# Performance work log

Hardware: AMD Instinct MI355X
Metric: run time of the kernel (lower is better)

## Reference

```python
import jax, jax.numpy as jnp
import numpy as np

N_W, N_E, N_UP, N_DN = 4096, 32, 16, 16
D, N_LAYERS, K_DET = 64, 3, 16
BOX = 6.0


def _ln(x, g, b, eps=1e-5):
    mu = x.mean(-1, keepdims=True)
    v = ((x - mu) ** 2).mean(-1, keepdims=True)
    return (x - mu) / jnp.sqrt(v + eps) * g + b


def setup_inputs() -> dict:
    key = jax.random.key(0)
    ks = jax.random.split(key, 24)
    f32 = jnp.float32

    def w(k, shape, s=0.1):
        return (jax.random.normal(k, shape) * s).astype(f32)

    cell = (BOX * jnp.eye(3)).astype(f32)
    twist = w(ks[0], (3,), 0.3)
    r_electrons = (jax.random.uniform(ks[1], (N_W, N_E, 3)) * BOX).astype(f32)
    inp = dict(
        r_electrons=r_electrons, cell=cell, twist=twist,
        W_e=w(ks[2], (3, D)), b_e=w(ks[3], (D,), 0.05),
        W_pw=w(ks[4], (6, D)), b_pw=w(ks[5], (D,), 0.05),
        W1=w(ks[6], (N_LAYERS, 3 * D, D)), b1=w(ks[7], (N_LAYERS, D), 0.05),
        W2=w(ks[8], (N_LAYERS, D, D)), b2=w(ks[9], (N_LAYERS, D), 0.05),
        ln_w=jnp.ones((N_LAYERS, D), f32), ln_b=jnp.zeros((N_LAYERS, D), f32),
        W_up=w(ks[10], (D, K_DET * N_UP)), b_up=w(ks[11], (K_DET * N_UP,), 0.05),
        W_dn=w(ks[12], (D, K_DET * N_DN)), b_dn=w(ks[13], (K_DET * N_DN,), 0.05),
        det_weights=jnp.zeros((K_DET,), f32),
        Wj1=w(ks[14], (1, 32)), bj1=w(ks[15], (32,), 0.05),
        Wj2=w(ks[16], (32, 32)), bj2=w(ks[17], (32,), 0.05),
        Wj3=w(ks[18], (32, 1)), bj3=w(ks[19], (1,), 0.05),
        jastrow_scale=jnp.asarray(0.1, f32),
    )
    return inp


def reference(r_electrons, cell, twist, W_e, b_e, W_pw, b_pw, W1, b1, W2, b2,
              ln_w, ln_b, W_up, b_up, W_dn, b_dn, det_weights,
              Wj1, bj1, Wj2, bj2, Wj3, bj3, jastrow_scale):
    L_inv = jnp.linalg.inv(cell)
    # wrap to cell via fractional coords
    s = r_electrons @ L_inv.T
    r = (s - jnp.floor(s)) @ cell  # [Nw, Ne, 3]
    # plane-wave features on wrapped positions
    s2 = r @ L_inv.T
    two_pi = 2.0 * jnp.pi
    pw = jnp.concatenate([jnp.sin(two_pi * s2), jnp.cos(two_pi * s2)], axis=-1)
    h = r @ W_e + b_e + pw @ W_pw + b_pw  # [Nw, Ne, D]
    # mean-field interaction layers
    for l in range(W1.shape[0]):
        hm = jnp.broadcast_to(h.mean(axis=1, keepdims=True), h.shape)
        x = jnp.concatenate([h, hm, h * hm], axis=-1)  # [Nw, Ne, 3D]
        delta = jax.nn.silu(x @ W1[l] + b1[l]) @ W2[l] + b2[l]
        h = _ln(h + delta, ln_w[l], ln_b[l])
    # minimum-image pairwise distances
    d = r[:, :, None, :] - r[:, None, :, :]  # [Nw, Ne, Ne, 3]
    sij = d @ L_inv.T
    vec = (sij - jnp.round(sij)) @ cell
    r_ij = jnp.linalg.norm(vec, axis=-1)  # [Nw, Ne, Ne]
    iu, ju = np.triu_indices(r.shape[1], 1)
    rp = r_ij[:, iu, ju][..., None]  # [Nw, P, 1]
    j = jax.nn.silu(rp @ Wj1 + bj1)
    j = jax.nn.silu(j @ Wj2 + bj2)
    j = (j @ Wj3 + bj3)[..., 0]
    jastrow = jastrow_scale * j.sum(axis=1)  # [Nw]
    # multi-determinant combine (vectorized over K via signed logsumexp)
    K = det_weights.shape[0]
    n_up = W_up.shape[1] // K
    n_dn = W_dn.shape[1] // K
    orb_up = h[:, :n_up] @ W_up + b_up  # [Nw, n_up, K*n_up]
    phi_up = jnp.moveaxis(orb_up.reshape(-1, n_up, K, n_up), 2, 1)  # [Nw,K,n_up,n_up]
    su, lu = jnp.linalg.slogdet(phi_up)
    orb_dn = h[:, n_up:] @ W_dn + b_dn
    phi_dn = jnp.moveaxis(orb_dn.reshape(-1, n_dn, K, n_dn), 2, 1)
    sd, ld = jnp.linalg.slogdet(phi_dn)
    logs = lu + ld + jnp.log(jax.nn.softmax(det_weights) + 1e-10)[None, :]  # [Nw,K]
    signs = su * sd
    m = jnp.max(logs, axis=1, keepdims=True)
    ssum = jnp.sum(signs * jnp.exp(logs - m), axis=1)
    log_psi = jastrow + m[:, 0] + jnp.log(jnp.abs(ssum) + 1e-30)
    sign_psi = jnp.sign(ssum)
    return log_psi, sign_psi
```

## Files before the change

kernel.cpp:

```cpp
#include <hip/hip_runtime.h>

#define N_WALK 4096
#define N_EL   32
#define DIM    64
#define HPAD   68
#define NLAY   3
#define KDET   16
#define NPAIR  496
#define TWO_PI_D 6.283185307179586476925286766559
#define JTAB_N    8192
#define JTAB_RMAX 5.25f

using f64x4 = __attribute__((ext_vector_type(4))) double;

#define MFMA64(A, B, C) __builtin_amdgcn_mfma_f64_16x16x4f64((A), (B), (C), 0, 0, 0)

__device__ __forceinline__ double exp_d(double x) {
  const double LOG2E  = 1.4426950408889634074;
  const double LN2_HI = 6.93147180369123816490e-01;
  const double LN2_LO = 1.90821492927058770002e-10;
  const double nf = rint(x * LOG2E);
  double r = fma(-nf, LN2_HI, x);
  r = fma(-nf, LN2_LO, r);
  double p = 1.0/3628800.0;
  p = fma(p, r, 1.0/362880.0);
  p = fma(p, r, 1.0/40320.0);
  p = fma(p, r, 1.0/5040.0);
  p = fma(p, r, 1.0/720.0);
  p = fma(p, r, 1.0/120.0);
  p = fma(p, r, 1.0/24.0);
  p = fma(p, r, 1.0/6.0);
  p = fma(p, r, 0.5);
  p = fma(p, r, 1.0);
  p = fma(p, r, 1.0);
  const long long bits = ((long long)((int)nf + 1023)) << 52;
  return p * __longlong_as_double(bits);
}

__device__ __forceinline__ double silu_d(double x) {
  const double d = 1.0 + exp_d(-x);
  const double q0 = (double)(1.0f / (float)d);
  double q = q0 * (2.0 - d * q0);
  q = q * (2.0 - d * q);
  return x * q;
}
__device__ __forceinline__ float silu_q(float x) { return x / (1.0f + __expf(-x)); }

__global__ __launch_bounds__(256) void jtab_kernel(
    const float* __restrict__ Wj1, const float* __restrict__ bj1,
    const float* __restrict__ Wj2, const float* __restrict__ bj2,
    const float* __restrict__ Wj3, const float* __restrict__ bj3,
    float* __restrict__ tab)
{
  const int i = blockIdx.x * 256 + threadIdx.x;
  if (i > JTAB_N) return;
  const float r = (float)i * (JTAB_RMAX / (float)JTAB_N);
  float h1[32];
  #pragma unroll
  for (int m=0;m<32;m++) h1[m] = silu_q(fmaf(r, Wj1[m], bj1[m]));
  float o = bj3[0];
  for (int n=0;n<32;n++) {
    float a2 = bj2[n];
    #pragma unroll
    for (int m=0;m<32;m++) a2 = fmaf(h1[m], Wj2[m*32+n], a2);
    o = fmaf(silu_q(a2), Wj3[n], o);
  }
  tab[i] = o;
}

__global__ __launch_bounds__(256) void wf_kernel(
    const float* __restrict__ r_el,
    const float* __restrict__ cell,
    const float* __restrict__ W_e,  const float* __restrict__ b_e,
    const float* __restrict__ W_pw, const float* __restrict__ b_pw,
    const float* __restrict__ W1,   const float* __restrict__ b1,
    const float* __restrict__ W2,   const float* __restrict__ b2,
    const float* __restrict__ ln_w, const float* __restrict__ ln_b,
    const float* __restrict__ W_up, const float* __restrict__ b_up,
    const float* __restrict__ W_dn, const float* __restrict__ b_dn,
    const float* __restrict__ det_w,
    const float* __restrict__ jtab,
    const float* __restrict__ jscale,
    float* __restrict__ out)
{
  __shared__ float s_linv[9];
  __shared__ float s_cl[9];
  __shared__ float s_r[N_EL][3];
  __shared__ float s_pw[N_EL][6];
  __shared__ float s_h[N_EL][HPAD];
  __shared__ float s_u[16*257];
  __shared__ float s_hm[DIM];
  __shared__ double s_hb[DIM];
  __shared__ double s_lu[2][KDET];
  __shared__ float  s_su[2][KDET];
  __shared__ float  s_red[4];
#define SY(e,d)   s_u[(e)*HPAD + (d)]
#define SORB(j,c) s_u[(j)*257 + (c)]

  const int t = threadIdx.x;
  const int w = blockIdx.x;
  const int wv = t >> 6;
  const int l  = t & 63;
  const int lr = l & 15;
  const int lq = l >> 4;

  if (t == 0) {
    double m00=cell[0], m01=cell[1], m02=cell[2];
    double m10=cell[3], m11=cell[4], m12=cell[5];
    double m20=cell[6], m21=cell[7], m22=cell[8];
    double c00 = m11*m22 - m12*m21;
    double c10 = m12*m20 - m10*m22;
    double c20 = m10*m21 - m11*m20;
    double det = m00*c00 + m01*c10 + m02*c20;
    double id = 1.0/det;
    s_linv[0]=(float)(c00*id); s_linv[1]=(float)((m02*m21-m01*m22)*id); s_linv[2]=(float)((m01*m12-m02*m11)*id);
    s_linv[3]=(float)(c10*id); s_linv[4]=(float)((m00*m22-m02*m20)*id); s_linv[5]=(float)((m02*m10-m00*m12)*id);
    s_linv[6]=(float)(c20*id); s_linv[7]=(float)((m01*m20-m00*m21)*id); s_linv[8]=(float)((m00*m11-m01*m10)*id);
    #pragma unroll
    for (int i=0;i<9;i++) s_cl[i]=cell[i];
  }
  __syncthreads();

  if (t < N_EL) {
    const float* rp = r_el + ((size_t)w * N_EL + t) * 3;
    const float rx = rp[0], ry = rp[1], rz = rp[2];
    float s0 = (float)((double)s_linv[0]*rx + (double)s_linv[1]*ry + (double)s_linv[2]*rz);
    float s1 = (float)((double)s_linv[3]*rx + (double)s_linv[4]*ry + (double)s_linv[5]*rz);
    float s2 = (float)((double)s_linv[6]*rx + (double)s_linv[7]*ry + (double)s_linv[8]*rz);
    s0 -= floorf(s0); s1 -= floorf(s1); s2 -= floorf(s2);
    const float wx = (float)((double)s0*s_cl[0] + (double)s1*s_cl[3] + (double)s2*s_cl[6]);
    const float wy = (float)((double)s0*s_cl[1] + (double)s1*s_cl[4] + (double)s2*s_cl[7]);
    const float wz = (float)((double)s0*s_cl[2] + (double)s1*s_cl[5] + (double)s2*s_cl[8]);
    s_r[t][0]=wx; s_r[t][1]=wy; s_r[t][2]=wz;
    const float u0 = (float)((double)s_linv[0]*wx + (double)s_linv[1]*wy + (double)s_linv[2]*wz);
    const float u1 = (float)((double)s_linv[3]*wx + (double)s_linv[4]*wy + (double)s_linv[5]*wz);
    const float u2 = (float)((double)s_linv[6]*wx + (double)s_linv[7]*wy + (double)s_linv[8]*wz);
    double sn, cs;
    sincos(TWO_PI_D*(double)u0, &sn, &cs); s_pw[t][0]=(float)sn; s_pw[t][3]=(float)cs;
    sincos(TWO_PI_D*(double)u1, &sn, &cs); s_pw[t][1]=(float)sn; s_pw[t][4]=(float)cs;
    sincos(TWO_PI_D*(double)u2, &sn, &cs); s_pw[t][2]=(float)sn; s_pw[t][5]=(float)cs;
  }
  __syncthreads();

  {
    const int e = t >> 3, db = (t & 7) * 8;
    const double rx=s_r[e][0], ry=s_r[e][1], rz=s_r[e][2];
    const double p0=s_pw[e][0],p1=s_pw[e][1],p2=s_pw[e][2];
    const double p3=s_pw[e][3],p4=s_pw[e][4],p5=s_pw[e][5];
    #pragma unroll
    for (int u=0;u<8;u++) {
      const int d = db+u;
      double acc = (double)b_e[d] + (double)b_pw[d];
      acc = fma(rx, (double)W_e[0*DIM+d], acc);
      acc = fma(ry, (double)W_e[1*DIM+d], acc);
      acc = fma(rz, (double)W_e[2*DIM+d], acc);
      acc = fma(p0, (double)W_pw[0*DIM+d], acc);
      acc = fma(p1, (double)W_pw[1*DIM+d], acc);
      acc = fma(p2, (double)W_pw[2*DIM+d], acc);
      acc = fma(p3, (double)W_pw[3*DIM+d], acc);
      acc = fma(p4, (double)W_pw[4*DIM+d], acc);
      acc = fma(p5, (double)W_pw[5*DIM+d], acc);
      s_h[e][d] = (float)acc;
    }
  }
  __syncthreads();

  const int m  = wv & 1;
  const int nb = (wv >> 1) * 2;
  const int ea = m*16 + lr;
  const int c0 = nb*16 + lr;
  const int er = m*16 + lq*4;

  for (int L = 0; L < NLAY; ++L) {
    const float* __restrict__ w1p = W1 + (size_t)L*192*DIM;
    const float* __restrict__ w2p = W2 + (size_t)L*DIM*DIM;

    if (t < DIM) {
      double s = 0.0;
      #pragma unroll 8
      for (int e=0;e<N_EL;e++) s += (double)s_h[e][t];
      const float hmf = (float)(s * (1.0/N_EL));
      s_hm[t] = hmf;
      double hb = (double)b1[L*DIM + t];
      #pragma unroll 8
      for (int km=0;km<DIM;km++)
        hb = fma((double)s_hm[km], (double)w1p[(64+km)*DIM + t], hb);
      s_hb[t] = hb;
    }
    __syncthreads();

    {
      f64x4 a0 = {0.0,0.0,0.0,0.0}, a1 = {0.0,0.0,0.0,0.0};
      #pragma unroll
      for (int kk=0;kk<16;kk++) {
        const int km = kk*4 + lq;
        const double af = (double)s_h[ea][km];
        const double q0 = (double)w1p[km*DIM + c0];
        const double q1 = (double)w1p[km*DIM + c0 + 16];
        a0 = MFMA64(af, q0, a0);
        a1 = MFMA64(af, q1, a1);
      }
      #pragma unroll
      for (int kk=0;kk<16;kk++) {
        const int km = kk*4 + lq;
        const double af = (double)(s_h[ea][km] * s_hm[km]);
        const double q0 = (double)w1p[(128+km)*DIM + c0];
        const double q1 = (double)w1p[(128+km)*DIM + c0 + 16];
        a0 = MFMA64(af, q0, a0);
        a1 = MFMA64(af, q1, a1);
      }
      #pragma unroll
      for (int v=0;v<4;v++) {
        const float p0 = (float)(a0[v] + s_hb[c0]);
        const float p1 = (float)(a1[v] + s_hb[c0 + 16]);
        SY(er+v, c0)      = (float)silu_d((double)p0);
        SY(er+v, c0 + 16) = (float)silu_d((double)p1);
      }
    }
    __syncthreads();

    {
      f64x4 a0 = {0.0,0.0,0.0,0.0}, a1 = {0.0,0.0,0.0,0.0};
      #pragma unroll
      for (int kk=0;kk<16;kk++) {
        const int km = kk*4 + lq;
        const double af = (double)SY(ea, km);
        const double q0 = (double)w2p[km*DIM + c0];
        const double q1 = (double)w2p[km*DIM + c0 + 16];
        a0 = MFMA64(af, q0, a0);
        a1 = MFMA64(af, q1, a1);
      }
      #pragma unroll
      for (int v=0;v<4;v++) {
        const float d0 = (float)(a0[v] + (double)b2[L*DIM + c0]);
        const float d1 = (float)(a1[v] + (double)b2[L*DIM + c0 + 16]);
        s_h[er+v][c0]      = s_h[er+v][c0]      + d0;
        s_h[er+v][c0 + 16] = s_h[er+v][c0 + 16] + d1;
      }
    }
    __syncthreads();

    {
      const int e = t >> 3, db = (t & 7) * 8;
      float v[8];
      double ps=0.0, pss=0.0;
      #pragma unroll
      for (int u=0;u<8;u++) {
        v[u] = s_h[e][db+u];
        ps += (double)v[u]; pss += (double)v[u]*(double)v[u];
      }
      #pragma unroll
      for (int off=4; off>=1; off>>=1) {
        ps  += __shfl_xor(ps,  off, 8);
        pss += __shfl_xor(pss, off, 8);
      }
      const double mu = ps * (1.0/DIM);
      double var = pss * (1.0/DIM) - mu*mu;
      var = fmax(var, 0.0);
      const double s = var + 1e-5;
      double rstd = (double)rsqrtf((float)s);
      rstd = rstd * (1.5 - 0.5*s*rstd*rstd);
      rstd = rstd * (1.5 - 0.5*s*rstd*rstd);
      #pragma unroll
      for (int u=0;u<8;u++) {
        const int d = db+u;
        s_h[e][d] = (float)(((double)v[u]-mu)*rstd*(double)ln_w[L*DIM+d] + (double)ln_b[L*DIM+d]);
      }
    }
    __syncthreads();
  }

  float jpart = 0.f;
  for (int p = t; p < NPAIR; p += 256) {
    int i = 0, rem = p;
    while (rem >= (N_EL-1) - i) { rem -= (N_EL-1) - i; ++i; }
    const int j = i + 1 + rem;
    const float dx = s_r[i][0]-s_r[j][0];
    const float dy = s_r[i][1]-s_r[j][1];
    const float dz = s_r[i][2]-s_r[j][2];
    float q0 = (float)((double)s_linv[0]*dx + (double)s_linv[1]*dy + (double)s_linv[2]*dz);
    float q1 = (float)((double)s_linv[3]*dx + (double)s_linv[4]*dy + (double)s_linv[5]*dz);
    float q2 = (float)((double)s_linv[6]*dx + (double)s_linv[7]*dy + (double)s_linv[8]*dz);
    q0 -= rintf(q0); q1 -= rintf(q1); q2 -= rintf(q2);
    const float vx = (float)((double)q0*s_cl[0] + (double)q1*s_cl[3] + (double)q2*s_cl[6]);
    const float vy = (float)((double)q0*s_cl[1] + (double)q1*s_cl[4] + (double)q2*s_cl[7]);
    const float vz = (float)((double)q0*s_cl[2] + (double)q1*s_cl[5] + (double)q2*s_cl[8]);
    const float rij = sqrtf(vx*vx + vy*vy + vz*vz);
    const float u = rij * ((float)JTAB_N / JTAB_RMAX);
    int i0 = (int)u;
    i0 = (i0 > JTAB_N-1) ? (JTAB_N-1) : i0;
    const float fr = u - (float)i0;
    const float f0 = jtab[i0], f1 = jtab[i0+1];
    jpart += fmaf(fr, f1 - f0, f0);
  }
  #pragma unroll
  for (int off=32; off>=1; off>>=1) jpart += __shfl_xor(jpart, off, 64);
  if ((t & 63) == 0) s_red[t >> 6] = jpart;

  {
    const int g4 = wv * 4;
    const int g  = t >> 4;
    const int r  = t & 15;
    double a0r[16], a1r[16];

    __builtin_amdgcn_s_setprio(1);
    #pragma unroll 1
    for (int gi=0; gi<4; ++gi) {
      const int cb = (g4 + gi)*16 + lr;
      f64x4 ac = {0.0,0.0,0.0,0.0};
      #pragma unroll
      for (int kk=0;kk<16;kk++) {
        const int km = kk*4 + lq;
        ac = MFMA64((double)s_h[lr][km], (double)W_up[(size_t)km*256 + cb], ac);
      }
      const int row = lq*4;
      #pragma unroll
      for (int v=0;v<4;v++)
        SORB(row+v, cb) = (float)(ac[v] + (double)b_up[cb]);
    }
    __builtin_amdgcn_s_setprio(0);
    #pragma unroll
    for (int j=0;j<16;j++) a0r[j] = (double)SORB(j, t);

    __builtin_amdgcn_s_setprio(1);
    #pragma unroll 1
    for (int gi=0; gi<4; ++gi) {
      const int cb = (g4 + gi)*16 + lr;
      f64x4 ac = {0.0,0.0,0.0,0.0};
      #pragma unroll
      for (int kk=0;kk<16;kk++) {
        const int km = kk*4 + lq;
        ac = MFMA64((double)s_h[16+lr][km], (double)W_dn[(size_t)km*256 + cb], ac);
      }
      const int row = lq*4;
      #pragma unroll
      for (int v=0;v<4;v++)
        SORB(row+v, cb) = (float)(ac[v] + (double)b_dn[cb]);
    }
    __builtin_amdgcn_s_setprio(0);
    #pragma unroll
    for (int j=0;j<16;j++) a1r[j] = (double)SORB(j, t);

    double prod0 = 1.0, prod1 = 1.0;
    int par0 = 0, par1 = 0;
    #pragma unroll
    for (int k=0;k<16;k++) {
      float bv0 = (r >= k) ? (float)fabs(a0r[k]) : -1.0f; int bi0 = r;
      float bv1 = (r >= k) ? (float)fabs(a1r[k]) : -1.0f; int bi1 = r;
      #pragma unroll
      for (int off=8; off>=1; off>>=1) {
        const float ov0 = __shfl_xor(bv0, off, 16); const int oi0 = __shfl_xor(bi0, off, 16);
        const float ov1 = __shfl_xor(bv1, off, 16); const int oi1 = __shfl_xor(bi1, off, 16);
        if (ov0 > bv0 || (ov0 == bv0 && oi0 < bi0)) { bv0 = ov0; bi0 = oi0; }
        if (ov1 > bv1 || (ov1 == bv1 && oi1 < bi1)) { bv1 = ov1; bi1 = oi1; }
      }
      const int p0 = bi0, p1 = bi1;
      par0 += (p0 != k) ? 1 : 0;
      par1 += (p1 != k) ? 1 : 0;
      const int src0 = (r == k) ? p0 : ((r == p0) ? k : r);
      const int src1 = (r == k) ? p1 : ((r == p1) ? k : r);
      const double piv0 = __shfl(a0r[k], p0, 16), nk0 = __shfl(a0r[k], src0, 16);
      const double piv1 = __shfl(a1r[k], p1, 16), nk1 = __shfl(a1r[k], src1, 16);
      prod0 *= piv0; prod1 *= piv1;
      const double f0 = (r > k && piv0 != 0.0) ? nk0/piv0 : 0.0;
      const double f1 = (r > k && piv1 != 0.0) ? nk1/piv1 : 0.0;
      a0r[k] = nk0; a1r[k] = nk1;
      #pragma unroll
      for (int j=k+1;j<16;j++) {
        const double sw0 = __shfl(a0r[j], src0, 16), kj0 = __shfl(a0r[j], p0, 16);
        const double sw1 = __shfl(a1r[j], src1, 16), kj1 = __shfl(a1r[j], p1, 16);
        a0r[j] = fma(-f0, kj0, sw0);
        a1r[j] = fma(-f1, kj1, sw1);
      }
    }
    if (r == 0) {
      s_lu[0][g] = log(fabs(prod0));
      s_su[0][g] = ((par0 + ((prod0 < 0.0) ? 1 : 0)) & 1) ? -1.f : 1.f;
      s_lu[1][g] = log(fabs(prod1));
      s_su[1][g] = ((par1 + ((prod1 < 0.0) ? 1 : 0)) & 1) ? -1.f : 1.f;
    }
  }
  __syncthreads();

  if (t < 16) {
    const int k = t;
    const double wwk = (double)det_w[k];
    double mw = wwk;
    #pragma unroll
    for (int off=8; off>=1; off>>=1) mw = fmax(mw, __shfl_xor(mw, off, 16));
    const double ew = exp_d(wwk - mw);
    double sum = ew;
    #pragma unroll
    for (int off=8; off>=1; off>>=1) sum += __shfl_xor(sum, off, 16);
    const double lg = s_lu[0][k] + s_lu[1][k] + log(ew/sum + 1e-10);
    const double sg = (double)(s_su[0][k] * s_su[1][k]);
    double m2 = lg;
    #pragma unroll
    for (int off=8; off>=1; off>>=1) m2 = fmax(m2, __shfl_xor(m2, off, 16));
    double ssum = sg * exp_d(lg - m2);
    #pragma unroll
    for (int off=8; off>=1; off>>=1) ssum += __shfl_xor(ssum, off, 16);
    if (t == 0) {
      const double jas = (double)jscale[0] * (double)(s_red[0]+s_red[1]+s_red[2]+s_red[3]);
      out[w] = (float)(jas + m2 + log(fabs(ssum) + 1e-30));
      out[N_WALK + w] = (ssum > 0.0) ? 1.f : ((ssum < 0.0) ? -1.f : 0.f);
    }
  }
}

extern "C" void kernel_launch(void* const* d_in, const int* in_sizes, int n_in,
                              void* d_out, int out_size, void* d_ws, size_t ws_size,
                              hipStream_t stream) {
  const float* r_el  = (const float*)d_in[0];
  const float* cell  = (const float*)d_in[1];
  const float* W_e   = (const float*)d_in[3];
  const float* b_e   = (const float*)d_in[4];
  const float* W_pw  = (const float*)d_in[5];
  const float* b_pw  = (const float*)d_in[6];
  const float* W1    = (const float*)d_in[7];
  const float* b1    = (const float*)d_in[8];
  const float* W2    = (const float*)d_in[9];
  const float* b2    = (const float*)d_in[10];
  const float* ln_w  = (const float*)d_in[11];
  const float* ln_b  = (const float*)d_in[12];
  const float* W_up  = (const float*)d_in[13];
  const float* b_up  = (const float*)d_in[14];
  const float* W_dn  = (const float*)d_in[15];
  const float* b_dn  = (const float*)d_in[16];
  const float* det_w = (const float*)d_in[17];
  const float* Wj1   = (const float*)d_in[18];
  const float* bj1   = (const float*)d_in[19];
  const float* Wj2   = (const float*)d_in[20];
  const float* bj2   = (const float*)d_in[21];
  const float* Wj3   = (const float*)d_in[22];
  const float* bj3   = (const float*)d_in[23];
  const float* jsc   = (const float*)d_in[24];
  float* jtab = (float*)d_ws;

  jtab_kernel<<<(JTAB_N + 1 + 255) / 256, 256, 0, stream>>>(
      Wj1, bj1, Wj2, bj2, Wj3, bj3, jtab);

  wf_kernel<<<N_WALK, 256, 0, stream>>>(
      r_el, cell, W_e, b_e, W_pw, b_pw, W1, b1, W2, b2, ln_w, ln_b,
      W_up, b_up, W_dn, b_dn, det_w, jtab, jsc,
      (float*)d_out);
}
```

Baseline: 493.9 us.

## Distribute mean-field bias per wave, parallelize sincos, drop a layer barrier

The per-layer mean and mean-field bias work, previously done by a single wave, is now done redundantly by every wave for the columns it owns. The K dimension is split across the two wave halves and the partial sums are combined with a cross-lane shuffle, which removes one __syncthreads per layer. The fp64 sincos for the plane-wave features now runs on 96 threads instead of 32, using scratch space inside s_u instead of a separate s_pw array. Row padding HPAD shrinks from 68 to 66, which changes the LDS bank mapping. The cost is redundant LDS writes of s_hm, and correctness now depends on wave-local LDS ordering without a barrier.

Measured after the change: 483.8 us. 2.0% less time.

```diff
diff --git a/kernel.cpp b/kernel.cpp
--- a/kernel.cpp
+++ b/kernel.cpp
@@ -3,7 +3,7 @@
 #define N_WALK 4096
 #define N_EL   32
 #define DIM    64
-#define HPAD   68
+#define HPAD   66
 #define NLAY   3
 #define KDET   16
 #define NPAIR  496
@@ -86,7 +86,6 @@
   __shared__ float s_linv[9];
   __shared__ float s_cl[9];
   __shared__ float s_r[N_EL][3];
-  __shared__ float s_pw[N_EL][6];
   __shared__ float s_h[N_EL][HPAD];
   __shared__ float s_u[16*257];
   __shared__ float s_hm[DIM];
@@ -95,6 +94,7 @@
   __shared__ float  s_su[2][KDET];
   __shared__ float  s_red[4];
 #define SY(e,d)   s_u[(e)*HPAD + (d)]
+#define SPW(e,i)  s_u[2112 + (e)*6 + (i)]
 #define SORB(j,c) s_u[(j)*257 + (c)]
 
   const int t = threadIdx.x;
@@ -132,21 +132,29 @@
     const float wy = (float)((double)s0*s_cl[1] + (double)s1*s_cl[4] + (double)s2*s_cl[7]);
     const float wz = (float)((double)s0*s_cl[2] + (double)s1*s_cl[5] + (double)s2*s_cl[8]);
     s_r[t][0]=wx; s_r[t][1]=wy; s_r[t][2]=wz;
-    const float u0 = (float)((double)s_linv[0]*wx + (double)s_linv[1]*wy + (double)s_linv[2]*wz);
-    const float u1 = (float)((double)s_linv[3]*wx + (double)s_linv[4]*wy + (double)s_linv[5]*wz);
-    const float u2 = (float)((double)s_linv[6]*wx + (double)s_linv[7]*wy + (double)s_linv[8]*wz);
-    double sn, cs;
-    sincos(TWO_PI_D*(double)u0, &sn, &cs); s_pw[t][0]=(float)sn; s_pw[t][3]=(float)cs;
-    sincos(TWO_PI_D*(double)u1, &sn, &cs); s_pw[t][1]=(float)sn; s_pw[t][4]=(float)cs;
-    sincos(TWO_PI_D*(double)u2, &sn, &cs); s_pw[t][2]=(float)sn; s_pw[t][5]=(float)cs;
+    SPW(t,0) = (float)((double)s_linv[0]*wx + (double)s_linv[1]*wy + (double)s_linv[2]*wz);
+    SPW(t,1) = (float)((double)s_linv[3]*wx + (double)s_linv[4]*wy + (double)s_linv[5]*wz);
+    SPW(t,2) = (float)((double)s_linv[6]*wx + (double)s_linv[7]*wy + (double)s_linv[8]*wz);
+  }
+  __syncthreads();
+
+  if (t < 128) {
+    const int e = t >> 2, ax = t & 3;
+    if (ax < 3) {
+      const float u = SPW(e, ax);
+      double sn, cs;
+      sincos(TWO_PI_D*(double)u, &sn, &cs);
+      SPW(e, ax)   = (float)sn;
+      SPW(e, ax+3) = (float)cs;
+    }
   }
   __syncthreads();
 
   {
     const int e = t >> 3, db = (t & 7) * 8;
     const double rx=s_r[e][0], ry=s_r[e][1], rz=s_r[e][2];
-    const double p0=s_pw[e][0],p1=s_pw[e][1],p2=s_pw[e][2];
-    const double p3=s_pw[e][3],p4=s_pw[e][4],p5=s_pw[e][5];
+    const double p0=SPW(e,0),p1=SPW(e,1),p2=SPW(e,2);
+    const double p3=SPW(e,3),p4=SPW(e,4),p5=SPW(e,5);
     #pragma unroll
     for (int u=0;u<8;u++) {
       const int d = db+u;
@@ -175,19 +183,21 @@
     const float* __restrict__ w1p = W1 + (size_t)L*192*DIM;
     const float* __restrict__ w2p = W2 + (size_t)L*DIM*DIM;
 
-    if (t < DIM) {
+    {
       double s = 0.0;
       #pragma unroll 8
-      for (int e=0;e<N_EL;e++) s += (double)s_h[e][t];
-      const float hmf = (float)(s * (1.0/N_EL));
-      s_hm[t] = hmf;
-      double hb = (double)b1[L*DIM + t];
+      for (int e=0;e<N_EL;e++) s += (double)s_h[e][l];
+      s_hm[l] = (float)(s * (1.0/N_EL));
+      const int c = nb*16 + (l & 31);
+      const int half = l >> 5;
+      double hb = (half == 0) ? (double)b1[L*DIM + c] : 0.0;
+      const int k0 = half*32;
       #pragma unroll 8
-      for (int km=0;km<DIM;km++)
-        hb = fma((double)s_hm[km], (double)w1p[(64+km)*DIM + t], hb);
-      s_hb[t] = hb;
-    }
-    __syncthreads();
+      for (int km=k0; km<k0+32; km++)
+        hb = fma((double)s_hm[km], (double)w1p[(64+km)*DIM + c], hb);
+      hb += __shfl_xor(hb, 32, 64);
+      if (half == 0) s_hb[c] = hb;
+    }
 
     {
       f64x4 a0 = {0.0,0.0,0.0,0.0}, a1 = {0.0,0.0,0.0,0.0};
```
